# Kernel tuning notes

Measured on AMD Instinct MI355X. Metric: run time of the kernel, lower is better.

Reference implementation:

```python
import jax, jax.numpy as jnp
import numpy as np

NUM_HEADS = 16
D_MODEL = 1024
SEQ = 4096
HEAD_DIM = D_MODEL // NUM_HEADS
ROPE_BASE = 10000.0


def _rope(x):
    # x: [h, s, d]  (rotate-half RoPE per head)
    s, d = x.shape[-2], x.shape[-1]
    inv_freq = 1.0 / (ROPE_BASE ** (jnp.arange(0, d, 2, dtype=jnp.float32) / d))  # [d/2]
    ang = jnp.arange(s, dtype=jnp.float32)[:, None] * inv_freq[None, :]           # [s, d/2]
    cos, sin = jnp.cos(ang), jnp.sin(ang)
    x1, x2 = x[..., : d // 2], x[..., d // 2 :]
    return jnp.concatenate([x1 * cos - x2 * sin, x1 * sin + x2 * cos], axis=-1)


def setup_inputs() -> dict:
    key = jax.random.key(0)
    kq, kk, kv, kwq, kwk, kwv = jax.random.split(key, 6)
    scale = 1.0 / np.sqrt(D_MODEL)
    return {
        "q": jax.random.normal(kq, (SEQ, D_MODEL), dtype=jnp.float32),
        "k": jax.random.normal(kk, (SEQ, D_MODEL), dtype=jnp.float32),
        "v": jax.random.normal(kv, (SEQ, D_MODEL), dtype=jnp.float32),
        "mask": jnp.tril(jnp.ones((SEQ, SEQ), dtype=bool)),  # causal
        "Wq": jax.random.normal(kwq, (D_MODEL, D_MODEL), dtype=jnp.float32) * scale,
        "Wk": jax.random.normal(kwk, (D_MODEL, D_MODEL), dtype=jnp.float32) * scale,
        "Wv": jax.random.normal(kwv, (D_MODEL, D_MODEL), dtype=jnp.float32) * scale,
    }


def reference(q, k, v, mask, Wq, Wk, Wv):
    # Projections (eqx Linear: x @ W.T, no bias)
    qp = q @ Wq.T  # [s, d_model]
    kp = k @ Wk.T
    vp = v @ Wv.T
    # split heads: [s, (h d)] -> [h, s, d]
    def split(x):
        return x.reshape(SEQ, NUM_HEADS, HEAD_DIM).transpose(1, 0, 2)
    qh, kh, vh = split(qp), split(kp), split(vp)
    qh = _rope(qh)
    kh = _rope(kh)
    # explicit full logits, masked softmax (matches original, no SDPA)
    logits = jnp.einsum("hqd,hkd->hqk", qh, kh) / jnp.sqrt(jnp.float32(HEAD_DIM))
    logits = jnp.where(mask[None, :, :], logits, -jnp.inf)
    attn = jax.nn.softmax(logits, axis=-1)  # [h, q, k]
    out = jnp.einsum("hqk,hkd->hqd", attn, vh)
    return out.transpose(1, 0, 2).reshape(SEQ, D_MODEL)
```

## Files before the change

kernel.cpp:

```cpp
#include <hip/hip_runtime.h>
#include <math.h>

#define SEQ 4096
#define DMODEL 1024
#define NHEADS 16
#define HDIM 64

typedef __bf16 v8bf __attribute__((ext_vector_type(8)));
typedef float f32x4 __attribute__((ext_vector_type(4)));
typedef float f32x16 __attribute__((ext_vector_type(16)));
typedef int i32x2 __attribute__((ext_vector_type(2)));
typedef int i32x4 __attribute__((ext_vector_type(4)));

#define NPART 4608
#define SCALE_Q 0.18033688011112042f

__device__ __forceinline__ unsigned short f2bf(float f) {
    union { float f; unsigned int u; } v; v.f = f;
    unsigned int u = v.u;
    return (unsigned short)((u + 0x7fffu + ((u >> 16) & 1u)) >> 16);
}

__device__ __forceinline__ int cvtpk(float lo, float hi) {
    int r;
    asm("v_cvt_pk_bf16_f32 %0, %1, %2" : "=v"(r) : "v"(lo), "v"(hi));
    return r;
}

__global__ __launch_bounds__(256) void proj_rope_kernel(
    const float* __restrict__ Xq, const float* __restrict__ Xk, const float* __restrict__ Xv,
    const float* __restrict__ Wq, const float* __restrict__ Wk, const float* __restrict__ Wv,
    unsigned short* __restrict__ qh, unsigned short* __restrict__ kh,
    unsigned short* __restrict__ vht)
{
    const int tz = blockIdx.z;
    const float* __restrict__ X = (tz == 0) ? Xq : (tz == 1) ? Xk : Xv;
    const float* __restrict__ W = (tz == 0) ? Wq : (tz == 1) ? Wk : Wv;

    const int tid = threadIdx.x;
    const int lane = tid & 63;
    const int wid = tid >> 6;
    const int l15 = lane & 15;
    const int l4 = lane >> 4;
    const int wr = wid >> 1, wc = wid & 1;

    const int m0 = blockIdx.x * 128;
    const int n0 = blockIdx.y * 128;

    __shared__ __align__(16) unsigned short Ab[128 * 32];
    __shared__ __align__(16) unsigned short Bb[128 * 32];

    float4 ra[4], rb[4];
    f32x4 acc[4][4] = {};

    #pragma unroll
    for (int c = 0; c < 4; ++c) {
        int i = tid + (c << 8);
        int row = i >> 3;
        int c4 = (i & 7) << 2;
        ra[c] = *reinterpret_cast<const float4*>(X + (size_t)(m0 + row) * DMODEL + c4);
        rb[c] = *reinterpret_cast<const float4*>(W + (size_t)(n0 + row) * DMODEL + c4);
    }

    for (int kt = 0; kt < 32; ++kt) {
        if (kt > 0) __syncthreads();
        #pragma unroll
        for (int c = 0; c < 4; ++c) {
            int i = tid + (c << 8);
            int row = i >> 3;
            int c4 = (i & 7) << 2;
            int byte = row * 64 + (((c4 >> 3) ^ ((row >> 1) & 3)) << 4) + ((c4 << 1) & 15);
            uint2 pa, pb;
            pa.x = (unsigned)f2bf(ra[c].x) | ((unsigned)f2bf(ra[c].y) << 16);
            pa.y = (unsigned)f2bf(ra[c].z) | ((unsigned)f2bf(ra[c].w) << 16);
            pb.x = (unsigned)f2bf(rb[c].x) | ((unsigned)f2bf(rb[c].y) << 16);
            pb.y = (unsigned)f2bf(rb[c].z) | ((unsigned)f2bf(rb[c].w) << 16);
            *reinterpret_cast<uint2*>(reinterpret_cast<char*>(Ab) + byte) = pa;
            *reinterpret_cast<uint2*>(reinterpret_cast<char*>(Bb) + byte) = pb;
        }
        if (kt < 31) {
            int k0 = (kt + 1) << 5;
            #pragma unroll
            for (int c = 0; c < 4; ++c) {
                int i = tid + (c << 8);
                int row = i >> 3;
                int c4 = (i & 7) << 2;
                ra[c] = *reinterpret_cast<const float4*>(X + (size_t)(m0 + row) * DMODEL + k0 + c4);
                rb[c] = *reinterpret_cast<const float4*>(W + (size_t)(n0 + row) * DMODEL + k0 + c4);
            }
        }
        __syncthreads();

        v8bf af[4], bfr[4];
        #pragma unroll
        for (int mi = 0; mi < 4; ++mi) {
            int row = wr * 64 + mi * 16 + l15;
            int byte = row * 64 + ((l4 ^ ((row >> 1) & 3)) << 4);
            af[mi] = *reinterpret_cast<const v8bf*>(reinterpret_cast<const char*>(Ab) + byte);
        }
        #pragma unroll
        for (int ni = 0; ni < 4; ++ni) {
            int row = wc * 64 + ni * 16 + l15;
            int byte = row * 64 + ((l4 ^ ((row >> 1) & 3)) << 4);
            bfr[ni] = *reinterpret_cast<const v8bf*>(reinterpret_cast<const char*>(Bb) + byte);
        }
        #pragma unroll
        for (int mi = 0; mi < 4; ++mi)
            #pragma unroll
            for (int ni = 0; ni < 4; ++ni)
                acc[mi][ni] = __builtin_amdgcn_mfma_f32_16x16x32_bf16(af[mi], bfr[ni], acc[mi][ni], 0, 0, 0);
    }

    const int h = (n0 >> 6) + wc;
    const int mbase = m0 + wr * 64;
    if (tz == 2) {
        unsigned short* base = vht + (size_t)h * HDIM * SEQ;
        #pragma unroll
        for (int mi = 0; mi < 4; ++mi) {
            #pragma unroll
            for (int ni = 0; ni < 4; ++ni) {
                int d = ni * 16 + l15;
                int m = mbase + mi * 16 + l4 * 4;
                uint2 pk;
                pk.x = (unsigned)f2bf(acc[mi][ni][0]) | ((unsigned)f2bf(acc[mi][ni][1]) << 16);
                pk.y = (unsigned)f2bf(acc[mi][ni][2]) | ((unsigned)f2bf(acc[mi][ni][3]) << 16);
                *reinterpret_cast<uint2*>(base + (size_t)d * SEQ + m) = pk;
            }
        }
    } else {
        unsigned short* base = ((tz == 0) ? qh : kh) + (size_t)h * SEQ * HDIM;
        const float scl = (tz == 0) ? SCALE_Q : 1.0f;
        #pragma unroll
        for (int ni = 0; ni < 2; ++ni) {
            int j = ni * 16 + l15;
            float invf = expf(-(float)j * 0.28782313662425574f);
            #pragma unroll
            for (int mi = 0; mi < 4; ++mi) {
                #pragma unroll
                for (int r = 0; r < 4; ++r) {
                    int m = mbase + mi * 16 + l4 * 4 + r;
                    float ang = (float)m * invf;
                    float sn, cs;
                    sincosf(ang, &sn, &cs);
                    sn *= scl; cs *= scl;
                    float x1 = acc[mi][ni][r];
                    float x2 = acc[mi][ni + 2][r];
                    base[(size_t)m * HDIM + j]      = f2bf(x1 * cs - x2 * sn);
                    base[(size_t)m * HDIM + j + 32] = f2bf(x1 * sn + x2 * cs);
                }
            }
        }
    }
}

__global__ __launch_bounds__(256) void repack_kernel(
    const unsigned short* __restrict__ kh, const unsigned short* __restrict__ vht,
    unsigned short* __restrict__ kfr, unsigned short* __restrict__ vfr)
{
    const int lane = threadIdx.x & 63;
    const int wid = threadIdx.x >> 6;
    const int l31 = lane & 31;
    const int l5 = lane >> 5;
    const int h = blockIdx.x >> 4;
    const int T = ((blockIdx.x & 15) << 2) + wid;

    const unsigned short* __restrict__ ksrc = kh + ((size_t)h * SEQ + T * 64) * HDIM;
    unsigned short* __restrict__ kdst = kfr + ((size_t)(h * 64 + T)) * 4096 + lane * 8;
    #pragma unroll
    for (int ns = 0; ns < 2; ++ns)
        #pragma unroll
        for (int dk = 0; dk < 4; ++dk) {
            v8bf f = *reinterpret_cast<const v8bf*>(ksrc + (ns * 32 + l31) * HDIM + dk * 16 + l5 * 8);
            *reinterpret_cast<v8bf*>(kdst + (ns * 4 + dk) * 512) = f;
        }

    const unsigned short* __restrict__ vsrc = vht + ((size_t)h * 64) * SEQ;
    unsigned short* __restrict__ vdst = vfr + ((size_t)(h * 64 + T)) * 4096 + lane * 8;
    #pragma unroll
    for (int dt = 0; dt < 2; ++dt)
        #pragma unroll
        for (int kb = 0; kb < 4; ++kb) {
            v8bf f = *reinterpret_cast<const v8bf*>(
                vsrc + (size_t)(dt * 32 + l31) * SEQ + T * 64 + kb * 16 + l5 * 8);
            *reinterpret_cast<v8bf*>(vdst + (dt * 4 + kb) * 512) = f;
        }
}

__global__ __launch_bounds__(64, 2) void attn_kernel(
    const unsigned short* __restrict__ qh, const unsigned short* __restrict__ kfr,
    const unsigned short* __restrict__ vfr, float* __restrict__ out,
    unsigned short* __restrict__ po, float* __restrict__ ml)
{
    const int lane = threadIdx.x & 63;
    const int l31 = lane & 31;
    const int l5 = lane >> 5;

    const int bid = blockIdx.x;
    const int xcd = bid & 7;
    const int idx = bid >> 3;
    const int hsel = (idx >= 320) ? 1 : 0;
    const int h = (xcd << 1) | hsel;
    const int r = 319 - (idx - hsel * 320);

    int qb, c, nc;
    if (r < 32)       { qb = r;                     c = 0;            nc = 1; }
    else if (r < 96)  { qb = 32 + ((r - 32) >> 1);  c = (r - 32) & 1; nc = 2; }
    else if (r < 192) { int rr = r - 96; qb = 64 + rr / 3; c = rr - (qb - 64) * 3; nc = 3; }
    else              { int rr = r - 192; qb = 96 + (rr >> 2); c = rr & 3; nc = 4; }

    const int q0 = qb * 32;
    const int q = q0 + l31;
    const int nt = (q0 + 32 + 63) >> 6;
    const int t0 = c * 16;
    const int t1 = min(t0 + 16, nt);

    const unsigned short* __restrict__ qbase = qh + ((size_t)h * SEQ + q) * HDIM + l5 * 8;
    const unsigned short* __restrict__ kfh = kfr + (size_t)h * 262144 + lane * 8;
    const unsigned short* __restrict__ vfh = vfr + (size_t)h * 262144 + lane * 8;

    v8bf qf[4];
    #pragma unroll
    for (int dk = 0; dk < 4; ++dk)
        qf[dk] = *reinterpret_cast<const v8bf*>(qbase + dk * 16);

    f32x16 of[2] = {};
    float mreg = -INFINITY, lreg = 0.0f;

    auto LOADK = [&](v8bf (&KB)[8], int T) {
        const unsigned short* kp = kfh + (size_t)T * 4096;
        #pragma unroll
        for (int f = 0; f < 8; ++f)
            KB[f] = *reinterpret_cast<const v8bf*>(kp + f * 512);
    };

    auto ROUND = [&](int T, v8bf (&KC)[8], v8bf (&KN)[8]) {
        v8bf vf[8];
        {
            const unsigned short* vp = vfh + (size_t)T * 4096;
            #pragma unroll
            for (int f = 0; f < 8; ++f)
                vf[f] = *reinterpret_cast<const v8bf*>(vp + f * 512);
        }
        if (T + 1 < t1) LOADK(KN, T + 1);

        f32x16 st[2];
        __builtin_amdgcn_s_setprio(1);
        #pragma unroll
        for (int ns = 0; ns < 2; ++ns) {
            f32x16 acc = {};
            #pragma unroll
            for (int dk = 0; dk < 4; ++dk)
                acc = __builtin_amdgcn_mfma_f32_32x32x16_bf16(KC[ns * 4 + dk], qf[dk], acc, 0, 0, 0);
            st[ns] = acc;
        }
        __builtin_amdgcn_s_setprio(0);

        if (T == nt - 1) {
            const int kvb = T * 64 + 4 * l5;
            #pragma unroll
            for (int ns = 0; ns < 2; ++ns)
                #pragma unroll
                for (int i = 0; i < 16; ++i) {
                    int kv = kvb + ns * 32 + (i & 3) + 8 * (i >> 2);
                    if (kv > q) st[ns][i] = -INFINITY;
                }
        }

        float t16[16];
        #pragma unroll
        for (int i = 0; i < 16; ++i) t16[i] = fmaxf(st[0][i], st[1][i]);
        #pragma unroll
        for (int i = 0; i < 8; ++i) t16[i] = fmaxf(t16[i], t16[i + 8]);
        #pragma unroll
        for (int i = 0; i < 4; ++i) t16[i] = fmaxf(t16[i], t16[i + 4]);
        float pmax = fmaxf(fmaxf(t16[0], t16[1]), fmaxf(t16[2], t16[3]));
        {
            i32x2 sw = __builtin_amdgcn_permlane32_swap(__float_as_int(pmax), __float_as_int(pmax), false, false);
            pmax = fmaxf(__int_as_float(sw.x), __int_as_float(sw.y));
        }

        if (!__all(pmax - mreg <= 8.0f)) {
            float mnew = fmaxf(mreg, pmax);
            float sc = exp2f(mreg - mnew);
            lreg *= sc;
            #pragma unroll
            for (int dt = 0; dt < 2; ++dt)
                #pragma unroll
                for (int i = 0; i < 16; ++i) of[dt][i] *= sc;
            mreg = mnew;
        }

        float ps0 = 0.f, ps1 = 0.f, ps2 = 0.f, ps3 = 0.f;
        #pragma unroll
        for (int ns = 0; ns < 2; ++ns)
            #pragma unroll
            for (int i = 0; i < 16; ++i) {
                float p = exp2f(st[ns][i] - mreg);
                st[ns][i] = p;
                if ((i & 3) == 0) ps0 += p; else if ((i & 3) == 1) ps1 += p;
                else if ((i & 3) == 2) ps2 += p; else ps3 += p;
            }
        lreg += (ps0 + ps1) + (ps2 + ps3);

        v8bf pt[4];
        #pragma unroll
        for (int kb = 0; kb < 4; ++kb) {
            int ns = kb >> 1, kp = (kb & 1) * 8;
            int A0 = cvtpk(st[ns][kp + 0], st[ns][kp + 1]);
            int A1 = cvtpk(st[ns][kp + 2], st[ns][kp + 3]);
            int B0 = cvtpk(st[ns][kp + 4], st[ns][kp + 5]);
            int B1 = cvtpk(st[ns][kp + 6], st[ns][kp + 7]);
            i32x2 s0 = __builtin_amdgcn_permlane32_swap(A0, B0, false, false);
            i32x2 s1 = __builtin_amdgcn_permlane32_swap(A1, B1, false, false);
            i32x4 u; u.x = s0.x; u.y = s1.x; u.z = s0.y; u.w = s1.y;
            v8bf p; __builtin_memcpy(&p, &u, 16);
            pt[kb] = p;
        }

        __builtin_amdgcn_s_setprio(1);
        #pragma unroll
        for (int dt = 0; dt < 2; ++dt)
            #pragma unroll
            for (int kb = 0; kb < 4; ++kb)
                of[dt] = __builtin_amdgcn_mfma_f32_32x32x16_bf16(vf[dt * 4 + kb], pt[kb], of[dt], 0, 0, 0);
        __builtin_amdgcn_s_setprio(0);
    };

    v8bf kA[8], kB[8];
    LOADK(kA, t0);
    int t = t0;
    while (true) {
        ROUND(t, kA, kB);
        if (++t == t1) break;
        ROUND(t, kB, kA);
        if (++t == t1) break;
    }

    {
        i32x2 sw = __builtin_amdgcn_permlane32_swap(__float_as_int(lreg), __float_as_int(lreg), false, false);
        lreg = __int_as_float(sw.x) + __int_as_float(sw.y);
    }

    if (nc == 1) {
        float inv = 1.0f / lreg;
        float* obase = out + (size_t)q * DMODEL + h * HDIM + l5 * 4;
        #pragma unroll
        for (int dt = 0; dt < 2; ++dt)
            #pragma unroll
            for (int g = 0; g < 4; ++g) {
                f32x4 o4;
                o4[0] = of[dt][g * 4 + 0] * inv;
                o4[1] = of[dt][g * 4 + 1] * inv;
                o4[2] = of[dt][g * 4 + 2] * inv;
                o4[3] = of[dt][g * 4 + 3] * inv;
                *reinterpret_cast<f32x4*>(obase + dt * 32 + g * 8) = o4;
            }
    } else {
        const int p = h * 288 + (r - 32);
        unsigned short* pb = po + ((size_t)p * 32 + l31) * 64 + l5 * 4;
        #pragma unroll
        for (int dt = 0; dt < 2; ++dt)
            #pragma unroll
            for (int g = 0; g < 4; ++g) {
                uint2 u;
                u.x = (unsigned)cvtpk(of[dt][g * 4 + 0], of[dt][g * 4 + 1]);
                u.y = (unsigned)cvtpk(of[dt][g * 4 + 2], of[dt][g * 4 + 3]);
                *reinterpret_cast<uint2*>(pb + dt * 32 + g * 8) = u;
            }
        if (l5 == 0) {
            float2 v; v.x = mreg; v.y = lreg;
            reinterpret_cast<float2*>(ml)[(size_t)p * 32 + l31] = v;
        }
    }
}

__global__ __launch_bounds__(256) void combine_kernel(
    const unsigned short* __restrict__ po, const float* __restrict__ ml,
    float* __restrict__ out)
{
    const int b = blockIdx.x;
    const int h = b / 96;
    const int j = b - h * 96;
    const int qb = 32 + j;
    int nc, r0;
    if (qb < 64)      { nc = 2; r0 = 32 + ((qb - 32) << 1); }
    else if (qb < 96) { nc = 3; r0 = 96 + (qb - 64) * 3; }
    else              { nc = 4; r0 = 192 + ((qb - 96) << 2); }
    const int p0 = h * 288 + (r0 - 32);
    const int d = threadIdx.x & 63;
    const int rg = threadIdx.x >> 6;
    const int q0 = qb * 32;

    for (int row = rg; row < 32; row += 4) {
        float mc[4], lc[4];
        float M = -INFINITY;
        #pragma unroll
        for (int ci = 0; ci < 4; ++ci)
            if (ci < nc) {
                float2 v = reinterpret_cast<const float2*>(ml)[(size_t)(p0 + ci) * 32 + row];
                mc[ci] = v.x; lc[ci] = v.y;
                M = fmaxf(M, v.x);
            }
        float L = 0.0f, O = 0.0f;
        #pragma unroll
        for (int ci = 0; ci < 4; ++ci)
            if (ci < nc) {
                float w = exp2f(mc[ci] - M);
                L += lc[ci] * w;
                unsigned int raw = po[((size_t)(p0 + ci) * 32 + row) * 64 + d];
                union { unsigned int u; float f; } cv; cv.u = raw << 16;
                O += cv.f * w;
            }
        out[(size_t)(q0 + row) * DMODEL + h * HDIM + d] = O / L;
    }
}

extern "C" void kernel_launch(void* const* d_in, const int* in_sizes, int n_in,
                              void* d_out, int out_size, void* d_ws, size_t ws_size,
                              hipStream_t stream) {
    (void)in_sizes; (void)n_in; (void)out_size; (void)ws_size;
    const float* q  = (const float*)d_in[0];
    const float* k  = (const float*)d_in[1];
    const float* v  = (const float*)d_in[2];
    const float* Wq = (const float*)d_in[4];
    const float* Wk = (const float*)d_in[5];
    const float* Wv = (const float*)d_in[6];

    unsigned short* qh  = (unsigned short*)d_ws;
    unsigned short* kfr = qh  + (size_t)NHEADS * SEQ * HDIM;
    unsigned short* vfr = kfr + (size_t)NHEADS * SEQ * HDIM;
    unsigned short* kh  = vfr + (size_t)NHEADS * SEQ * HDIM;
    unsigned short* vht = kh  + (size_t)NHEADS * SEQ * HDIM;
    unsigned short* po  = kh;
    float* ml = (float*)(po + (size_t)NPART * 32 * 64);
    float* out = (float*)d_out;

    dim3 g1(SEQ / 128, DMODEL / 128, 3);
    proj_rope_kernel<<<g1, 256, 0, stream>>>(q, k, v, Wq, Wk, Wv, qh, kh, vht);

    repack_kernel<<<dim3(256), 256, 0, stream>>>(kh, vht, kfr, vfr);

    attn_kernel<<<dim3(16 * 320), 64, 0, stream>>>(qh, kfr, vfr, out, po, ml);

    combine_kernel<<<dim3(16 * 96), 256, 0, stream>>>(po, ml, out);
}
```

Before: 163.0 us.

## Load projection tiles directly to LDS as fp32 and convert at fragment read

The projection GEMM now uses global_load_lds to copy fp32 tiles of X and W straight into shared memory with an XOR-swizzled layout. Conversion to bf16 moves from the store path to the fragment read path, using packed cvt instructions. This removes the register staging and the manual bf16 conversion before LDS stores. In exchange it doubles LDS footprint and read traffic, converts the same data more than once (each tile is read by two waves), and drops the register prefetch of the next k-tile, so global latency is no longer overlapped with MFMA work.

```diff
diff --git a/kernel.cpp b/kernel.cpp
--- a/kernel.cpp
+++ b/kernel.cpp
@@ -25,6 +25,12 @@
     int r;
     asm("v_cvt_pk_bf16_f32 %0, %1, %2" : "=v"(r) : "v"(lo), "v"(hi));
     return r;
+}
+
+__device__ __forceinline__ void gload16(const float* g, float* l) {
+    __builtin_amdgcn_global_load_lds(
+        (const __attribute__((address_space(1))) float*)g,
+        (__attribute__((address_space(3))) float*)l, 16, 0, 0);
 }
 
 __global__ __launch_bounds__(256) void proj_rope_kernel(
@@ -47,47 +53,31 @@
     const int m0 = blockIdx.x * 128;
     const int n0 = blockIdx.y * 128;
 
-    __shared__ __align__(16) unsigned short Ab[128 * 32];
-    __shared__ __align__(16) unsigned short Bb[128 * 32];
-
-    float4 ra[4], rb[4];
-    f32x4 acc[4][4] = {};
-
+    __shared__ __align__(16) float Ab[128 * 32];
+    __shared__ __align__(16) float Bb[128 * 32];
+
+    int rowc[4], colc[4];
     #pragma unroll
     for (int c = 0; c < 4; ++c) {
-        int i = tid + (c << 8);
-        int row = i >> 3;
-        int c4 = (i & 7) << 2;
-        ra[c] = *reinterpret_cast<const float4*>(X + (size_t)(m0 + row) * DMODEL + c4);
-        rb[c] = *reinterpret_cast<const float4*>(W + (size_t)(n0 + row) * DMODEL + c4);
-    }
+        int row = wid * 32 + c * 8 + (lane >> 3);
+        int blk = (lane & 7) ^ (row & 7);
+        rowc[c] = row;
+        colc[c] = blk * 4;
+    }
+
+    f32x4 acc[4][4] = {};
 
     for (int kt = 0; kt < 32; ++kt) {
         if (kt > 0) __syncthreads();
+        const int k0 = kt << 5;
         #pragma unroll
         for (int c = 0; c < 4; ++c) {
-            int i = tid + (c << 8);
-            int row = i >> 3;
-            int c4 = (i & 7) << 2;
-            int byte = row * 64 + (((c4 >> 3) ^ ((row >> 1) & 3)) << 4) + ((c4 << 1) & 15);
-            uint2 pa, pb;
-            pa.x = (unsigned)f2bf(ra[c].x) | ((unsigned)f2bf(ra[c].y) << 16);
-            pa.y = (unsigned)f2bf(ra[c].z) | ((unsigned)f2bf(ra[c].w) << 16);
-            pb.x = (unsigned)f2bf(rb[c].x) | ((unsigned)f2bf(rb[c].y) << 16);
-            pb.y = (unsigned)f2bf(rb[c].z) | ((unsigned)f2bf(rb[c].w) << 16);
-            *reinterpret_cast<uint2*>(reinterpret_cast<char*>(Ab) + byte) = pa;
-            *reinterpret_cast<uint2*>(reinterpret_cast<char*>(Bb) + byte) = pb;
-        }
-        if (kt < 31) {
-            int k0 = (kt + 1) << 5;
-            #pragma unroll
-            for (int c = 0; c < 4; ++c) {
-                int i = tid + (c << 8);
-                int row = i >> 3;
-                int c4 = (i & 7) << 2;
-                ra[c] = *reinterpret_cast<const float4*>(X + (size_t)(m0 + row) * DMODEL + k0 + c4);
-                rb[c] = *reinterpret_cast<const float4*>(W + (size_t)(n0 + row) * DMODEL + k0 + c4);
-            }
+            const float* ga = X + (size_t)(m0 + rowc[c]) * DMODEL + k0 + colc[c];
+            const float* gb = W + (size_t)(n0 + rowc[c]) * DMODEL + k0 + colc[c];
+            float* la = Ab + (wid * 1024 + c * 256);
+            float* lb = Bb + (wid * 1024 + c * 256);
+            gload16(ga, la);
+            gload16(gb, lb);
         }
         __syncthreads();
 
@@ -95,14 +85,26 @@
         #pragma unroll
         for (int mi = 0; mi < 4; ++mi) {
             int row = wr * 64 + mi * 16 + l15;
-            int byte = row * 64 + ((l4 ^ ((row >> 1) & 3)) << 4);
-            af[mi] = *reinterpret_cast<const v8bf*>(reinterpret_cast<const char*>(Ab) + byte);
+            const char* base = reinterpret_cast<const char*>(Ab) + row * 128;
+            f32x4 lo = *reinterpret_cast<const f32x4*>(base + ((((l4 << 1)    ) ^ (row & 7)) << 4));
+            f32x4 hi = *reinterpret_cast<const f32x4*>(base + ((((l4 << 1) | 1) ^ (row & 7)) << 4));
+            i32x4 u;
+            u.x = cvtpk(lo[0], lo[1]); u.y = cvtpk(lo[2], lo[3]);
+            u.z = cvtpk(hi[0], hi[1]); u.w = cvtpk(hi[2], hi[3]);
+            v8bf r; __builtin_memcpy(&r, &u, 16);
+            af[mi] = r;
         }
         #pragma unroll
         for (int ni = 0; ni < 4; ++ni) {
             int row = wc * 64 + ni * 16 + l15;
-            int byte = row * 64 + ((l4 ^ ((row >> 1) & 3)) << 4);
-            bfr[ni] = *reinterpret_cast<const v8bf*>(reinterpret_cast<const char*>(Bb) + byte);
+            const char* base = reinterpret_cast<const char*>(Bb) + row * 128;
+            f32x4 lo = *reinterpret_cast<const f32x4*>(base + ((((l4 << 1)    ) ^ (row & 7)) << 4));
+            f32x4 hi = *reinterpret_cast<const f32x4*>(base + ((((l4 << 1) | 1) ^ (row & 7)) << 4));
+            i32x4 u;
+            u.x = cvtpk(lo[0], lo[1]); u.y = cvtpk(lo[2], lo[3]);
+            u.z = cvtpk(hi[0], hi[1]); u.w = cvtpk(hi[2], hi[3]);
+            v8bf r; __builtin_memcpy(&r, &u, 16);
+            bfr[ni] = r;
         }
         #pragma unroll
         for (int mi = 0; mi < 4; ++mi)
```

Measured after the change: 175.0 us. +7.3%, slower.

## Double-buffer LDS tiles in QKV projection GEMM and use packed bf16 conversion

Applied to the files above, without the earlier changes.

The projection GEMM now keeps two shared-memory buffers for the A and B tiles. The next tile's global loads are issued before the MFMA work on the current buffer and written into the other buffer afterwards, which removes one barrier per k-step and lets the loads overlap compute. The scalar float-to-bf16 rounding is replaced by the packed cvtpk helper, both for staging and for the V output. This doubles LDS use per block, which may lower occupancy.

```diff
diff --git a/kernel.cpp b/kernel.cpp
--- a/kernel.cpp
+++ b/kernel.cpp
@@ -47,68 +47,75 @@
     const int m0 = blockIdx.x * 128;
     const int n0 = blockIdx.y * 128;
 
-    __shared__ __align__(16) unsigned short Ab[128 * 32];
-    __shared__ __align__(16) unsigned short Bb[128 * 32];
-
-    float4 ra[4], rb[4];
-    f32x4 acc[4][4] = {};
-
+    __shared__ __align__(16) unsigned short Ab[2][128 * 32];
+    __shared__ __align__(16) unsigned short Bb[2][128 * 32];
+
+    int srow[4], sc4[4], sbyte[4];
     #pragma unroll
     for (int c = 0; c < 4; ++c) {
         int i = tid + (c << 8);
         int row = i >> 3;
         int c4 = (i & 7) << 2;
-        ra[c] = *reinterpret_cast<const float4*>(X + (size_t)(m0 + row) * DMODEL + c4);
-        rb[c] = *reinterpret_cast<const float4*>(W + (size_t)(n0 + row) * DMODEL + c4);
-    }
+        srow[c] = row; sc4[c] = c4;
+        sbyte[c] = row * 64 + (((c4 >> 3) ^ ((row >> 1) & 3)) << 4) + ((c4 << 1) & 15);
+    }
+
+    float4 ra[4], rb[4];
+
+    auto GLOAD = [&](int kt) {
+        const int k0 = kt << 5;
+        #pragma unroll
+        for (int c = 0; c < 4; ++c) {
+            ra[c] = *reinterpret_cast<const float4*>(X + (size_t)(m0 + srow[c]) * DMODEL + k0 + sc4[c]);
+            rb[c] = *reinterpret_cast<const float4*>(W + (size_t)(n0 + srow[c]) * DMODEL + k0 + sc4[c]);
+        }
+    };
+    auto PACKW = [&](int b) {
+        #pragma unroll
+        for (int c = 0; c < 4; ++c) {
+            uint2 pa, pb;
+            pa.x = (unsigned)cvtpk(ra[c].x, ra[c].y);
+            pa.y = (unsigned)cvtpk(ra[c].z, ra[c].w);
+            pb.x = (unsigned)cvtpk(rb[c].x, rb[c].y);
+            pb.y = (unsigned)cvtpk(rb[c].z, rb[c].w);
+            *reinterpret_cast<uint2*>(reinterpret_cast<char*>(Ab[b]) + sbyte[c]) = pa;
+            *reinterpret_cast<uint2*>(reinterpret_cast<char*>(Bb[b]) + sbyte[c]) = pb;
+        }
+    };
+
+    f32x4 acc[4][4] = {};
+
+    GLOAD(0);
+    PACKW(0);
 
     for (int kt = 0; kt < 32; ++kt) {
-        if (kt > 0) __syncthreads();
-        #pragma unroll
-        for (int c = 0; c < 4; ++c) {
-            int i = tid + (c << 8);
-            int row = i >> 3;
-            int c4 = (i & 7) << 2;
-            int byte = row * 64 + (((c4 >> 3) ^ ((row >> 1) & 3)) << 4) + ((c4 << 1) & 15);
-            uint2 pa, pb;
-            pa.x = (unsigned)f2bf(ra[c].x) | ((unsigned)f2bf(ra[c].y) << 16);
-            pa.y = (unsigned)f2bf(ra[c].z) | ((unsigned)f2bf(ra[c].w) << 16);
-            pb.x = (unsigned)f2bf(rb[c].x) | ((unsigned)f2bf(rb[c].y) << 16);
-            pb.y = (unsigned)f2bf(rb[c].z) | ((unsigned)f2bf(rb[c].w) << 16);
-            *reinterpret_cast<uint2*>(reinterpret_cast<char*>(Ab) + byte) = pa;
-            *reinterpret_cast<uint2*>(reinterpret_cast<char*>(Bb) + byte) = pb;
-        }
-        if (kt < 31) {
-            int k0 = (kt + 1) << 5;
-            #pragma unroll
-            for (int c = 0; c < 4; ++c) {
-                int i = tid + (c << 8);
-                int row = i >> 3;
-                int c4 = (i & 7) << 2;
-                ra[c] = *reinterpret_cast<const float4*>(X + (size_t)(m0 + row) * DMODEL + k0 + c4);
-                rb[c] = *reinterpret_cast<const float4*>(W + (size_t)(n0 + row) * DMODEL + k0 + c4);
-            }
-        }
         __syncthreads();
+        const bool hn = (kt < 31);
+        if (hn) GLOAD(kt + 1);
+
+        const unsigned short* A = Ab[kt & 1];
+        const unsigned short* B = Bb[kt & 1];
 
         v8bf af[4], bfr[4];
         #pragma unroll
         for (int mi = 0; mi < 4; ++mi) {
             int row = wr * 64 + mi * 16 + l15;
             int byte = row * 64 + ((l4 ^ ((row >> 1) & 3)) << 4);
-            af[mi] = *reinterpret_cast<const v8bf*>(reinterpret_cast<const char*>(Ab) + byte);
+            af[mi] = *reinterpret_cast<const v8bf*>(reinterpret_cast<const char*>(A) + byte);
         }
         #pragma unroll
         for (int ni = 0; ni < 4; ++ni) {
             int row = wc * 64 + ni * 16 + l15;
             int byte = row * 64 + ((l4 ^ ((row >> 1) & 3)) << 4);
-            bfr[ni] = *reinterpret_cast<const v8bf*>(reinterpret_cast<const char*>(Bb) + byte);
+            bfr[ni] = *reinterpret_cast<const v8bf*>(reinterpret_cast<const char*>(B) + byte);
         }
         #pragma unroll
         for (int mi = 0; mi < 4; ++mi)
             #pragma unroll
             for (int ni = 0; ni < 4; ++ni)
                 acc[mi][ni] = __builtin_amdgcn_mfma_f32_16x16x32_bf16(af[mi], bfr[ni], acc[mi][ni], 0, 0, 0);
+
+        if (hn) PACKW((kt + 1) & 1);
     }
 
     const int h = (n0 >> 6) + wc;
@@ -122,8 +129,8 @@
                 int d = ni * 16 + l15;
                 int m = mbase + mi * 16 + l4 * 4;
                 uint2 pk;
-                pk.x = (unsigned)f2bf(acc[mi][ni][0]) | ((unsigned)f2bf(acc[mi][ni][1]) << 16);
-                pk.y = (unsigned)f2bf(acc[mi][ni][2]) | ((unsigned)f2bf(acc[mi][ni][3]) << 16);
+                pk.x = (unsigned)cvtpk(acc[mi][ni][0], acc[mi][ni][1]);
+                pk.y = (unsigned)cvtpk(acc[mi][ni][2], acc[mi][ni][3]);
                 *reinterpret_cast<uint2*>(base + (size_t)d * SEQ + m) = pk;
             }
         }
```

Measured after the change: 161.5 us. No clear change (-0.9%).
